# Performance work log

Measured on AMD Instinct MI355X. Metric: run time of the kernel, lower is better.

## Reference

```python
import jax, jax.numpy as jnp
import numpy as np

T_MAX = 4
TOP_K = 4
TEMP = 1.0
THRESH = 0.99
EPS = 1e-6


def _to_c(x):
    return x[..., 0] + 1j * x[..., 1]


def _from_c(z):
    return jnp.stack([z.real, z.imag], axis=-1)


def _forward(psi, bank_keys, bank_vals, u_halt, W_halt, b_halt, head_mix, out_scale):
    B, T, d, _ = psi.shape
    H = bank_keys.shape[0]
    psi_flat = psi.reshape(B * T, d, 2)
    BT = psi_flat.shape[0]
    psi_h = jnp.broadcast_to(psi_flat[:, None], (BT, H, d, 2))
    cum = jnp.zeros((BT, H), psi.dtype)
    halted = jnp.zeros((BT, H), bool)
    cost = jnp.zeros((BT, H), psi.dtype)
    acc = jnp.zeros((BT, H, d, 2), psi.dtype)
    # normalized halt target vectors u (OrthoHalt)
    uc = _to_c(u_halt)  # [H,d] complex
    un = uc / jnp.sqrt(jnp.sum(uc.real**2 + uc.imag**2, -1, keepdims=True) + EPS)
    hidx = jnp.arange(H)
    for it in range(T_MAX):  # fixed small reasoning depth (structural loop)
        is_last = it == T_MAX - 1
        psi_pool = psi_h.mean(axis=1)                       # [BT,d,2]
        feat = psi_pool.reshape(BT, 2 * d)
        # effect-bank probe + top-k gather
        scores = jnp.einsum('bf,hnf->bhn', feat, bank_keys) / TEMP
        w = jax.nn.softmax(scores, axis=-1)                 # [BT,H,N]
        topw, topi = jax.lax.top_k(w, TOP_K)                # [BT,H,K]
        vecs = bank_vals[hidx[None, :, None], topi]         # [BT,H,K,d,2]
        U = _to_c(vecs) * topw[..., None].astype(jnp.complex64)  # weighted basis
        # rank-K Sasaki projection: Pi_F psi = A (A^H A)^{-1} A^H psi, A = U^T
        psic = _to_c(psi_h)                                 # [BT,H,d]
        m = jnp.einsum('bhkd,bhd->bhk', jnp.conj(U), psic)
        G = jnp.einsum('bhkd,bhjd->bhkj', jnp.conj(U), U)
        G = G + EPS * jnp.eye(TOP_K, dtype=G.dtype)
        coeff = jnp.linalg.solve(G, m[..., None])[..., 0]
        proj = jnp.einsum('bhkd,bhk->bhd', U, coeff)
        psi_next = _from_c(proj)
        # renormalize_psi
        sq = (psi_next[..., 0] ** 2 + psi_next[..., 1] ** 2).sum(-1, keepdims=True)
        psi_next = psi_next / jnp.sqrt(jnp.maximum(sq, 1e-6))[..., None]
        # OrthoHalt on pooled next state -> (alpha, beta, gamma) -> 3 logits
        pool_next = _to_c(psi_next.mean(axis=1))            # [BT,d]
        c = jnp.einsum('hd,bd->bh', jnp.conj(un), pool_next)
        ns = jnp.sum(pool_next.real**2 + pool_next.imag**2, -1)[:, None] + EPS
        alpha = (c.real**2 + c.imag**2) / ns
        beta = 1.0 - alpha
        gamma = c.real**2 / ns
        abg = jnp.stack([alpha, beta, gamma], -1)           # [BT,H,3]
        logits = jnp.einsum('bhi,hij->bhj', abg, W_halt) + b_halt
        probs = jax.nn.softmax(logits, -1)
        p_halt = probs[..., 0] + probs[..., 1]              # yes + no mass
        # ACT ponder update
        would = cum + p_halt
        halts_now = jnp.logical_or(would >= THRESH, is_last)
        active = jnp.logical_not(halted)
        weight = jnp.where(active, jnp.where(halts_now, 1.0 - cum, p_halt), 0.0)
        cost = cost + jnp.where(active, p_halt, 0.0)
        cum = jnp.where(jnp.logical_and(active, jnp.logical_not(halts_now)), would, cum)
        halted = jnp.logical_or(halted, jnp.logical_and(active, halts_now))
        acc = acc + weight[..., None, None] * psi_next
        psi_h = psi_next
    head_w = jax.nn.softmax(head_mix)[None, :, None, None]
    merged = (acc * head_w).sum(axis=1)                     # [BT,d,2]
    residual = merged - psi_flat
    psi_out = (psi_flat + out_scale * residual).reshape(B, T, d, 2)
    return psi_out, cost.mean()


def setup_inputs() -> dict:
    key = jax.random.key(0)
    ks = jax.random.split(key, 6)
    B, T, d, H, N = 2, 2048, 512, 4, 2048
    psi = jax.random.normal(ks[0], (B, T, d, 2), jnp.float32)
    psi = psi / jnp.sqrt(jnp.maximum((psi**2).sum((-1, -2), keepdims=True), 1e-6))
    bank_keys = 0.05 * jax.random.normal(ks[1], (H, N, 2 * d), jnp.float32)
    bank_vals = jax.random.normal(ks[2], (H, N, d, 2), jnp.float32)
    u_halt = jax.random.normal(ks[3], (H, d, 2), jnp.float32)
    W_halt = jax.random.normal(ks[4], (H, 3, 3), jnp.float32)
    b_halt = jnp.zeros((H, 3), jnp.float32)
    head_mix = jnp.zeros((H,), jnp.float32)
    out_scale = jnp.asarray(0.1, jnp.float32)
    return dict(psi=psi, bank_keys=bank_keys, bank_vals=bank_vals, u_halt=u_halt,
                W_halt=W_halt, b_halt=b_halt, head_mix=head_mix, out_scale=out_scale)


def reference(psi, bank_keys, bank_vals, u_halt, W_halt, b_halt, head_mix, out_scale):
    return _forward(psi, bank_keys, bank_vals, u_halt, W_halt, b_halt, head_mix, out_scale)
```

## Files before the change

kernel.cpp:

```cpp
#include <hip/hip_runtime.h>
#include <math.h>

#define HH 4
#define DD 512
#define FF 1024
#define NN 2048
#define KK 4
#define TMAXI 4
#define THRESHV 0.99f
#define EPSV 1e-6f

typedef unsigned short ushort_t;
typedef __attribute__((ext_vector_type(8))) __bf16 bf16x8;
typedef __attribute__((ext_vector_type(8))) _Float16 half8;
typedef __attribute__((ext_vector_type(4))) float f32x4;
typedef __attribute__((ext_vector_type(4))) unsigned short us4;

__device__ __forceinline__ unsigned short f2bf(float x) {
    unsigned int u = __float_as_uint(x);
    unsigned int r = (u + 0x7FFF + ((u >> 16) & 1)) >> 16;
    return (unsigned short)r;
}

__device__ __forceinline__ float fast_rcp(float x) { return __builtin_amdgcn_rcpf(x); }

typedef __attribute__((address_space(3))) unsigned int lds_u32;
typedef __attribute__((address_space(1))) const unsigned int glb_u32;
__device__ __forceinline__ void gl_lds16(const void* g, void* s) {
    __builtin_amdgcn_global_load_lds((glb_u32*)g, (lds_u32*)s, 16, 0, 0);
}

__global__ void k_unorm(const float* __restrict__ u_halt, float* __restrict__ norm_inv) {
    __shared__ float red[256];
    int tid = threadIdx.x;
    for (int h = 0; h < HH; ++h) {
        float s = 0.f;
        for (int i = tid; i < FF; i += 256) { float v = u_halt[h * FF + i]; s += v * v; }
        red[tid] = s; __syncthreads();
        for (int off = 128; off > 0; off >>= 1) {
            if (tid < off) red[tid] += red[tid + off];
            __syncthreads();
        }
        if (tid == 0) norm_inv[h] = 1.0f / sqrtf(red[0] + EPSV);
        __syncthreads();
    }
}

__global__ void k_cvt_bf(const float* __restrict__ in, ushort_t* __restrict__ out, int total) {
    int i = blockIdx.x * 256 + threadIdx.x;
    if (i >= total) return;
    out[i] = f2bf(in[i]);
}

#define BM 128
#define BN 128
#define BKE 64
__global__ __launch_bounds__(256) void k_gemm_mfma(const ushort_t* __restrict__ A,
                                                   const ushort_t* __restrict__ B,
                                                   ushort_t* __restrict__ C) {
    __shared__ __align__(16) ushort_t As[BM * BKE];
    __shared__ __align__(16) ushort_t Bs[BN * BKE];
    int tid = threadIdx.x;
    int lane = tid & 63, w = tid >> 6;
    int row0 = blockIdx.y * BM, col0 = blockIdx.x * BN;

    int srow = lane >> 3;
    int schunk = (lane & 7) ^ srow;
    const ushort_t* gA = A + (size_t)(row0 + w * 32 + srow) * FF + schunk * 8;
    const ushort_t* gB = B + (size_t)(col0 + w * 32 + srow) * FF + schunk * 8;
    ushort_t* sA = As + (w * 32) * BKE;
    ushort_t* sB = Bs + (w * 32) * BKE;

    int fr = lane & 15;
    int q  = lane >> 4;
    int wr0 = (w >> 1) * 64, wc0 = (w & 1) * 64;

    f32x4 acc[4][4] = {};

    for (int kb = 0; kb < FF; kb += BKE) {
        #pragma unroll
        for (int i = 0; i < 4; i++) {
            gl_lds16(gA + kb + (size_t)(8 * i) * FF, sA + (8 * i) * BKE);
            gl_lds16(gB + kb + (size_t)(8 * i) * FF, sB + (8 * i) * BKE);
        }
        __syncthreads();
        bf16x8 af[2][4], bfv[2][4];
        #pragma unroll
        for (int hf = 0; hf < 2; hf++) {
            int ck = ((4 * hf + q) ^ (fr & 7)) * 8;
            #pragma unroll
            for (int i = 0; i < 4; i++) {
                af[hf][i]  = *(const bf16x8*)&As[(wr0 + 16 * i + fr) * BKE + ck];
                bfv[hf][i] = *(const bf16x8*)&Bs[(wc0 + 16 * i + fr) * BKE + ck];
            }
        }
        #pragma unroll
        for (int hf = 0; hf < 2; hf++)
            #pragma unroll
            for (int i = 0; i < 4; i++)
                #pragma unroll
                for (int j = 0; j < 4; j++)
                    acc[i][j] = __builtin_amdgcn_mfma_f32_16x16x32_bf16(af[hf][i], bfv[hf][j], acc[i][j], 0, 0, 0);
        __syncthreads();
    }

    int crow = (lane >> 4) * 4;
    int ccol = lane & 15;
    #pragma unroll
    for (int i = 0; i < 4; i++)
        #pragma unroll
        for (int r = 0; r < 4; r++) {
            ushort_t* Cr = C + (size_t)(row0 + wr0 + 16 * i + crow + r) * (HH * NN) + col0 + wc0 + ccol;
            #pragma unroll
            for (int j = 0; j < 4; j++) {
                _Float16 hv = (_Float16)acc[i][j][r];
                Cr[16 * j] = *(ushort_t*)&hv;
            }
        }
}

__global__ __launch_bounds__(256) void k_softtop(const ushort_t* __restrict__ Sc,
                                                 float* __restrict__ topw, int* __restrict__ topi,
                                                 int row0) {
    int tid = threadIdx.x;
    int w = tid >> 6, lane = tid & 63;
    int g = blockIdx.x * 4 + w;
    int r = g >> 2;
    int h = g & 3;
    const ushort_t* S = Sc + (size_t)r * (HH * NN) + h * NN + lane * 8;
    float f0[8], f1[8], f2[8], f3[8];
    {
        half8 h0 = *(const half8*)(S);
        half8 h1 = *(const half8*)(S + 512);
        half8 h2 = *(const half8*)(S + 1024);
        half8 h3 = *(const half8*)(S + 1536);
        #pragma unroll
        for (int e = 0; e < 8; e++) {
            f0[e] = (float)h0[e]; f1[e] = (float)h1[e];
            f2[e] = (float)h2[e]; f3[e] = (float)h3[e];
        }
    }

    float bm = f0[0];
    #pragma unroll
    for (int e = 0; e < 8; e++) {
        bm = fmaxf(bm, fmaxf(fmaxf(f0[e], f1[e]), fmaxf(f2[e], f3[e])));
    }
    #pragma unroll
    for (int m = 1; m < 64; m <<= 1) bm = fmaxf(bm, __shfl_xor(bm, m, 64));

    float se = 0.f;
    #pragma unroll
    for (int e = 0; e < 8; e++)
        se += __expf(f0[e] - bm) + __expf(f1[e] - bm) + __expf(f2[e] - bm) + __expf(f3[e] - bm);
    #pragma unroll
    for (int m = 1; m < 64; m <<= 1) se += __shfl_xor(se, m, 64);
    float Zinv = fast_rcp(se);

    int gbh = (row0 + r) * HH + h;
    int base = lane * 8;
    #pragma unroll
    for (int k = 0; k < KK; k++) {
        float bv = -INFINITY; int bi = NN;
        #pragma unroll
        for (int e = 0; e < 8; e++) {
            if (f0[e] > bv) { bv = f0[e]; bi = base + e; }
        }
        #pragma unroll
        for (int e = 0; e < 8; e++) {
            if (f1[e] > bv) { bv = f1[e]; bi = 512 + base + e; }
        }
        #pragma unroll
        for (int e = 0; e < 8; e++) {
            if (f2[e] > bv) { bv = f2[e]; bi = 1024 + base + e; }
        }
        #pragma unroll
        for (int e = 0; e < 8; e++) {
            if (f3[e] > bv) { bv = f3[e]; bi = 1536 + base + e; }
        }
        #pragma unroll
        for (int m = 1; m < 64; m <<= 1) {
            float ov = __shfl_xor(bv, m, 64);
            int   oi = __shfl_xor(bi, m, 64);
            if (ov > bv || (ov == bv && oi < bi)) { bv = ov; bi = oi; }
        }
        if (lane == 0) {
            topw[gbh * KK + k] = __expf(bv - bm) * Zinv;
            topi[gbh * KK + k] = bi;
        }
        if (k < KK - 1) {
            #pragma unroll
            for (int e = 0; e < 8; e++) {
                if (base + e == bi)        f0[e] = -INFINITY;
                if (512 + base + e == bi)  f1[e] = -INFINITY;
                if (1024 + base + e == bi) f2[e] = -INFINITY;
                if (1536 + base + e == bi) f3[e] = -INFINITY;
            }
        }
    }
}

__global__ __launch_bounds__(256) void k_fused(const float* __restrict__ psi,
                                               float* __restrict__ psi_h,
                                               const float* __restrict__ bank_vals,
                                               const float* __restrict__ topw,
                                               const int* __restrict__ topi,
                                               const float* __restrict__ u_halt,
                                               const float* __restrict__ norm_inv,
                                               const float* __restrict__ W_halt,
                                               const float* __restrict__ b_halt,
                                               const float* __restrict__ head_mix,
                                               float* __restrict__ merged,
                                               ushort_t* __restrict__ feat,
                                               float* __restrict__ cum,
                                               float* __restrict__ cost,
                                               int* __restrict__ halted,
                                               int first, int is_last) {
    __shared__ float Pn[HH][FF];
    __shared__ float xw[4][9];
    int b = blockIdx.x;
    int tid = threadIdx.x;
    int w = tid >> 6, lane = tid & 63;
    int bh = b * HH + w;

    float wk[KK]; int ix[KK];
    #pragma unroll
    for (int k = 0; k < KK; k++) { wk[k] = topw[bh * KK + k]; ix[k] = topi[bh * KK + k]; }

    const float* Pr = first ? (psi + (size_t)b * FF) : (psi_h + (size_t)bh * FF);
    float4 p4[4], v4[KK][4];
    #pragma unroll
    for (int c = 0; c < 4; c++) p4[c] = *(const float4*)(Pr + lane * 16 + 4 * c);
    #pragma unroll
    for (int k = 0; k < KK; k++) {
        const float* Vp = bank_vals + ((size_t)(w * NN) + ix[k]) * FF + lane * 16;
        #pragma unroll
        for (int c = 0; c < 4; c++) v4[k][c] = *(const float4*)(Vp + 4 * c);
    }

    float part[24];
    #pragma unroll
    for (int t = 0; t < 24; t++) part[t] = 0.f;
    #pragma unroll
    for (int c = 0; c < 4; c++) {
        #pragma unroll
        for (int e = 0; e < 2; e++) {
            float prr = e ? p4[c].z : p4[c].x;
            float pii = e ? p4[c].w : p4[c].y;
            float vr[KK], vi[KK];
            #pragma unroll
            for (int k = 0; k < KK; k++) {
                vr[k] = e ? v4[k][c].z : v4[k][c].x;
                vi[k] = e ? v4[k][c].w : v4[k][c].y;
            }
            #pragma unroll
            for (int k = 0; k < KK; k++) {
                part[2 * k]     += vr[k] * prr + vi[k] * pii;
                part[2 * k + 1] += vr[k] * pii - vi[k] * prr;
                part[8 + k]     += vr[k] * vr[k] + vi[k] * vi[k];
            }
            int t = 12;
            #pragma unroll
            for (int k = 0; k < KK; k++)
                #pragma unroll
                for (int j = k + 1; j < KK; j++) {
                    part[t]     += vr[k] * vr[j] + vi[k] * vi[j];
                    part[t + 1] += vr[k] * vi[j] - vi[k] * vr[j];
                    t += 2;
                }
        }
    }
    #pragma unroll
    for (int m = 1; m < 64; m <<= 1)
        #pragma unroll
        for (int t = 0; t < 24; t++) part[t] += __shfl_xor(part[t], m, 64);

    float mr[KK], mi[KK], Gr[KK][KK], Gi[KK][KK];
    #pragma unroll
    for (int k = 0; k < KK; k++) {
        mr[k] = part[2 * k] * wk[k];
        mi[k] = part[2 * k + 1] * wk[k];
        Gr[k][k] = part[8 + k] * wk[k] * wk[k] + EPSV;
        Gi[k][k] = 0.f;
    }
    {
        int t = 12;
        #pragma unroll
        for (int k = 0; k < KK; k++)
            #pragma unroll
            for (int j = k + 1; j < KK; j++) {
                float s = wk[k] * wk[j];
                Gr[k][j] = part[t] * s;  Gi[k][j] = part[t + 1] * s;
                Gr[j][k] = Gr[k][j];     Gi[j][k] = -Gi[k][j];
                t += 2;
            }
    }

    float Lr[KK][KK], Li[KK][KK];
    #pragma unroll
    for (int j = 0; j < KK; j++) {
        float s = Gr[j][j];
        #pragma unroll
        for (int p = 0; p < KK; p++) if (p < j) s -= Lr[j][p] * Lr[j][p] + Li[j][p] * Li[j][p];
        float ljj = sqrtf(fmaxf(s, 1e-30f));
        Lr[j][j] = ljj; Li[j][j] = 0.f;
        float inv = 1.0f / ljj;
        #pragma unroll
        for (int k = 0; k < KK; k++) {
            if (k > j) {
                float ar = Gr[k][j], ai = Gi[k][j];
                #pragma unroll
                for (int p = 0; p < KK; p++) if (p < j) {
                    ar -= Lr[k][p] * Lr[j][p] + Li[k][p] * Li[j][p];
                    ai -= Li[k][p] * Lr[j][p] - Lr[k][p] * Li[j][p];
                }
                Lr[k][j] = ar * inv; Li[k][j] = ai * inv;
            }
        }
    }
    float yr[KK], yi[KK];
    #pragma unroll
    for (int j = 0; j < KK; j++) {
        float ar = mr[j], ai = mi[j];
        #pragma unroll
        for (int p = 0; p < KK; p++) if (p < j) {
            ar -= Lr[j][p] * yr[p] - Li[j][p] * yi[p];
            ai -= Lr[j][p] * yi[p] + Li[j][p] * yr[p];
        }
        float inv = 1.0f / Lr[j][j];
        yr[j] = ar * inv; yi[j] = ai * inv;
    }
    float xr[KK], xi2[KK];
    #pragma unroll
    for (int j = KK - 1; j >= 0; j--) {
        float ar = yr[j], ai = yi[j];
        #pragma unroll
        for (int p = 0; p < KK; p++) if (p > j) {
            ar -= Lr[p][j] * xr[p] + Li[p][j] * xi2[p];
            ai -= Lr[p][j] * xi2[p] - Li[p][j] * xr[p];
        }
        float inv = 1.0f / Lr[j][j];
        xr[j] = ar * inv; xi2[j] = ai * inv;
    }
    float cxr[KK], cxi[KK];
    #pragma unroll
    for (int k = 0; k < KK; k++) { cxr[k] = xr[k] * wk[k]; cxi[k] = xi2[k] * wk[k]; }

    float4 pj[4];
    float sqp = 0.f;
    #pragma unroll
    for (int c = 0; c < 4; c++) {
        float ar0 = 0.f, ai0 = 0.f, ar1 = 0.f, ai1 = 0.f;
        #pragma unroll
        for (int k = 0; k < KK; k++) {
            ar0 += v4[k][c].x * cxr[k] - v4[k][c].y * cxi[k];
            ai0 += v4[k][c].x * cxi[k] + v4[k][c].y * cxr[k];
            ar1 += v4[k][c].z * cxr[k] - v4[k][c].w * cxi[k];
            ai1 += v4[k][c].z * cxi[k] + v4[k][c].w * cxr[k];
        }
        pj[c].x = ar0; pj[c].y = ai0; pj[c].z = ar1; pj[c].w = ai1;
        sqp += ar0 * ar0 + ai0 * ai0 + ar1 * ar1 + ai1 * ai1;
    }
    #pragma unroll
    for (int m = 1; m < 64; m <<= 1) sqp += __shfl_xor(sqp, m, 64);
    float rn = 1.0f / sqrtf(fmaxf(sqp, 1e-6f));

    float* Pdst = psi_h + (size_t)bh * FF + lane * 16;
    #pragma unroll
    for (int c = 0; c < 4; c++) {
        float4 o; o.x = pj[c].x * rn; o.y = pj[c].y * rn; o.z = pj[c].z * rn; o.w = pj[c].w * rn;
        if (!is_last) *(float4*)(Pdst + 4 * c) = o;
        *(float4*)&Pn[w][lane * 16 + 4 * c] = o;
    }
    __syncthreads();

    int t4 = tid * 4;
    float4 a0 = *(const float4*)&Pn[0][t4];
    float4 a1 = *(const float4*)&Pn[1][t4];
    float4 a2 = *(const float4*)&Pn[2][t4];
    float4 a3 = *(const float4*)&Pn[3][t4];
    float4 pool;
    pool.x = 0.25f * (a0.x + a1.x + a2.x + a3.x);
    pool.y = 0.25f * (a0.y + a1.y + a2.y + a3.y);
    pool.z = 0.25f * (a0.z + a1.z + a2.z + a3.z);
    pool.w = 0.25f * (a0.w + a1.w + a2.w + a3.w);

    float pt[9];
    #pragma unroll
    for (int h = 0; h < HH; h++) {
        float4 u = *(const float4*)&u_halt[h * FF + t4];
        pt[2 * h]     = u.x * pool.x + u.y * pool.y + u.z * pool.z + u.w * pool.w;
        pt[2 * h + 1] = u.x * pool.y - u.y * pool.x + u.z * pool.w - u.w * pool.z;
    }
    pt[8] = pool.x * pool.x + pool.y * pool.y + pool.z * pool.z + pool.w * pool.w;
    #pragma unroll
    for (int m = 1; m < 64; m <<= 1)
        #pragma unroll
        for (int t = 0; t < 9; t++) pt[t] += __shfl_xor(pt[t], m, 64);
    if (lane == 0) {
        #pragma unroll
        for (int t = 0; t < 9; t++) xw[w][t] = pt[t];
    }
    __syncthreads();
    float red[9];
    #pragma unroll
    for (int t = 0; t < 9; t++) red[t] = xw[0][t] + xw[1][t] + xw[2][t] + xw[3][t];
    float ns = red[8] + EPSV;

    float hm0 = head_mix[0], hm1 = head_mix[1], hm2 = head_mix[2], hm3 = head_mix[3];
    float hmx = fmaxf(fmaxf(hm0, hm1), fmaxf(hm2, hm3));
    float he[4] = {expf(hm0 - hmx), expf(hm1 - hmx), expf(hm2 - hmx), expf(hm3 - hmx)};
    float hsum = he[0] + he[1] + he[2] + he[3];

    float wgt[4], addc[4], newcum[4]; int newhl[4];
    int idxb = b * HH;
    #pragma unroll
    for (int h = 0; h < HH; h++) {
        float cr = red[2 * h] * norm_inv[h], ci = red[2 * h + 1] * norm_inv[h];
        float alpha = (cr * cr + ci * ci) / ns;
        float beta = 1.0f - alpha;
        float gamma = cr * cr / ns;
        float lg[3];
        #pragma unroll
        for (int j = 0; j < 3; j++)
            lg[j] = alpha * W_halt[(h * 3 + 0) * 3 + j] + beta * W_halt[(h * 3 + 1) * 3 + j] +
                    gamma * W_halt[(h * 3 + 2) * 3 + j] + b_halt[h * 3 + j];
        float mx = fmaxf(lg[0], fmaxf(lg[1], lg[2]));
        float e0 = expf(lg[0] - mx), e1 = expf(lg[1] - mx), e2 = expf(lg[2] - mx);
        float p_halt = (e0 + e1) / (e0 + e1 + e2);
        float cm = cum[idxb + h];
        int hl = halted[idxb + h];
        float would = cm + p_halt;
        int halts_now = (would >= THRESHV) || is_last;
        int active = hl ? 0 : 1;
        wgt[h]  = active ? (halts_now ? (1.0f - cm) : p_halt) : 0.0f;
        addc[h] = active ? p_halt : 0.0f;
        newcum[h] = (active && !halts_now) ? would : cm;
        newhl[h]  = hl || (active && halts_now);
    }
    __syncthreads();
    if (tid < HH) {
        cost[idxb + tid] += addc[tid];
        cum[idxb + tid] = newcum[tid];
        halted[idxb + tid] = newhl[tid];
    }
    float hwv[4];
    #pragma unroll
    for (int h = 0; h < HH; h++) hwv[h] = (he[h] / hsum) * wgt[h];

    size_t mo = (size_t)b * FF + t4;
    float4 m4 = *(const float4*)&merged[mo];
    m4.x += hwv[0] * a0.x + hwv[1] * a1.x + hwv[2] * a2.x + hwv[3] * a3.x;
    m4.y += hwv[0] * a0.y + hwv[1] * a1.y + hwv[2] * a2.y + hwv[3] * a3.y;
    m4.z += hwv[0] * a0.z + hwv[1] * a1.z + hwv[2] * a2.z + hwv[3] * a3.z;
    m4.w += hwv[0] * a0.w + hwv[1] * a1.w + hwv[2] * a2.w + hwv[3] * a3.w;
    *(float4*)&merged[mo] = m4;

    if (!is_last) {
        us4 fb;
        fb.x = f2bf(pool.x); fb.y = f2bf(pool.y); fb.z = f2bf(pool.z); fb.w = f2bf(pool.w);
        *(us4*)&feat[mo] = fb;
    }
}

__global__ void k_out(const float* __restrict__ psi, const float* __restrict__ merged,
                      const float* __restrict__ out_scale, float* __restrict__ out, int total) {
    int i = blockIdx.x * 256 + threadIdx.x;
    if (i >= total) return;
    float p = psi[i];
    out[i] = p + out_scale[0] * (merged[i] - p);
}

__global__ void k_costmean(const float* __restrict__ cost, float* __restrict__ out, int n) {
    __shared__ float red[256];
    int tid = threadIdx.x;
    float s = 0.f;
    for (int i = tid; i < n; i += 256) s += cost[i];
    red[tid] = s; __syncthreads();
    for (int off = 128; off > 0; off >>= 1) {
        if (tid < off) red[tid] += red[tid + off];
        __syncthreads();
    }
    if (tid == 0) out[0] = red[0] / (float)n;
}

extern "C" void kernel_launch(void* const* d_in, const int* in_sizes, int n_in,
                              void* d_out, int out_size, void* d_ws, size_t ws_size,
                              hipStream_t stream) {
    const float* psi       = (const float*)d_in[0];
    const float* bank_keys = (const float*)d_in[1];
    const float* bank_vals = (const float*)d_in[2];
    const float* u_halt    = (const float*)d_in[3];
    const float* W_halt    = (const float*)d_in[4];
    const float* b_halt    = (const float*)d_in[5];
    const float* head_mix  = (const float*)d_in[6];
    const float* out_scale = (const float*)d_in[7];
    float* out = (float*)d_out;

    const int BT = in_sizes[0] / FF;

    float* ws = (float*)d_ws;
    size_t off = 0;
    float* psi_h  = ws + off; off += (size_t)BT * HH * FF;
    float* merged = ws + off; off += (size_t)BT * FF;
    float* cum    = ws + off; off += (size_t)BT * HH;
    float* costv  = ws + off; off += (size_t)BT * HH;
    int*   halted = (int*)(ws + off); off += (size_t)BT * HH;
    float* topw   = ws + off; off += (size_t)BT * HH * KK;
    int*   topi   = (int*)(ws + off); off += (size_t)BT * HH * KK;
    float* norminv = ws + off; off += 16;
    ushort_t* feat_bf = (ushort_t*)(ws + off); off += (size_t)BT * FF / 2;
    ushort_t* keys_bf = (ushort_t*)(ws + off); off += (size_t)HH * NN * FF / 2;
    ushort_t* scores = (ushort_t*)(ws + off);
    size_t fixed = off;

    size_t ws_floats = ws_size / 4;
    int RC = BT;
    while (RC > 128 && fixed + (size_t)RC * HH * NN / 2 > ws_floats) RC >>= 1;
    int nchunks = BT / RC;

    hipMemsetAsync(merged, 0, ((size_t)BT * FF + 3 * (size_t)BT * HH) * sizeof(float), stream);
    k_unorm<<<1, 256, 0, stream>>>(u_halt, norminv);
    int tot_keys = HH * NN * FF;
    k_cvt_bf<<<(tot_keys + 255) / 256, 256, 0, stream>>>(bank_keys, keys_bf, tot_keys);
    int tot_bf = BT * FF;
    k_cvt_bf<<<(tot_bf + 255) / 256, 256, 0, stream>>>(psi, feat_bf, tot_bf);

    for (int it = 0; it < TMAXI; ++it) {
        for (int c = 0; c < nchunks; ++c) {
            k_gemm_mfma<<<dim3((HH * NN) / BN, RC / BM), 256, 0, stream>>>(
                feat_bf + (size_t)c * RC * FF, keys_bf, scores);
            k_softtop<<<dim3((RC * HH) / 4), 256, 0, stream>>>(scores, topw, topi, c * RC);
        }
        k_fused<<<BT, 256, 0, stream>>>(psi, psi_h, bank_vals, topw, topi, u_halt, norminv,
                                        W_halt, b_halt, head_mix, merged, feat_bf,
                                        cum, costv, halted,
                                        (it == 0) ? 1 : 0, (it == TMAXI - 1) ? 1 : 0);
    }
    k_out<<<(tot_bf + 255) / 256, 256, 0, stream>>>(psi, merged, out_scale, out, tot_bf);
    k_costmean<<<1, 256, 0, stream>>>(costv, out + tot_bf, BT * HH);
}
```

Before: 1.056 ms.

## Fuse softmax/top-k into the fused step kernel, vectorize bf16 conversion, drop chunking

Moves the softmax and top-k selection from a separate kernel into the start of k_fused, so each wave reads its score row directly and keeps the top-k weights and indices in registers. This removes one launch per iteration and the topw/topi global round trip. The bf16 conversion kernel now handles four floats per thread, and the score GEMM always runs over all rows at once instead of in workspace-limited chunks. Dropping the chunking assumes the workspace can hold the full BT x H x N score buffer; if it cannot, the writes overflow it.

```diff
diff --git a/kernel.cpp b/kernel.cpp
--- a/kernel.cpp
+++ b/kernel.cpp
@@ -46,10 +46,13 @@
     }
 }
 
-__global__ void k_cvt_bf(const float* __restrict__ in, ushort_t* __restrict__ out, int total) {
+__global__ void k_cvt_bf4(const float* __restrict__ in, ushort_t* __restrict__ out, int total4) {
     int i = blockIdx.x * 256 + threadIdx.x;
-    if (i >= total) return;
-    out[i] = f2bf(in[i]);
+    if (i >= total4) return;
+    float4 v = ((const float4*)in)[i];
+    us4 o;
+    o.x = f2bf(v.x); o.y = f2bf(v.y); o.z = f2bf(v.z); o.w = f2bf(v.w);
+    ((us4*)out)[i] = o;
 }
 
 #define BM 128
@@ -119,92 +122,10 @@
         }
 }
 
-__global__ __launch_bounds__(256) void k_softtop(const ushort_t* __restrict__ Sc,
-                                                 float* __restrict__ topw, int* __restrict__ topi,
-                                                 int row0) {
-    int tid = threadIdx.x;
-    int w = tid >> 6, lane = tid & 63;
-    int g = blockIdx.x * 4 + w;
-    int r = g >> 2;
-    int h = g & 3;
-    const ushort_t* S = Sc + (size_t)r * (HH * NN) + h * NN + lane * 8;
-    float f0[8], f1[8], f2[8], f3[8];
-    {
-        half8 h0 = *(const half8*)(S);
-        half8 h1 = *(const half8*)(S + 512);
-        half8 h2 = *(const half8*)(S + 1024);
-        half8 h3 = *(const half8*)(S + 1536);
-        #pragma unroll
-        for (int e = 0; e < 8; e++) {
-            f0[e] = (float)h0[e]; f1[e] = (float)h1[e];
-            f2[e] = (float)h2[e]; f3[e] = (float)h3[e];
-        }
-    }
-
-    float bm = f0[0];
-    #pragma unroll
-    for (int e = 0; e < 8; e++) {
-        bm = fmaxf(bm, fmaxf(fmaxf(f0[e], f1[e]), fmaxf(f2[e], f3[e])));
-    }
-    #pragma unroll
-    for (int m = 1; m < 64; m <<= 1) bm = fmaxf(bm, __shfl_xor(bm, m, 64));
-
-    float se = 0.f;
-    #pragma unroll
-    for (int e = 0; e < 8; e++)
-        se += __expf(f0[e] - bm) + __expf(f1[e] - bm) + __expf(f2[e] - bm) + __expf(f3[e] - bm);
-    #pragma unroll
-    for (int m = 1; m < 64; m <<= 1) se += __shfl_xor(se, m, 64);
-    float Zinv = fast_rcp(se);
-
-    int gbh = (row0 + r) * HH + h;
-    int base = lane * 8;
-    #pragma unroll
-    for (int k = 0; k < KK; k++) {
-        float bv = -INFINITY; int bi = NN;
-        #pragma unroll
-        for (int e = 0; e < 8; e++) {
-            if (f0[e] > bv) { bv = f0[e]; bi = base + e; }
-        }
-        #pragma unroll
-        for (int e = 0; e < 8; e++) {
-            if (f1[e] > bv) { bv = f1[e]; bi = 512 + base + e; }
-        }
-        #pragma unroll
-        for (int e = 0; e < 8; e++) {
-            if (f2[e] > bv) { bv = f2[e]; bi = 1024 + base + e; }
-        }
-        #pragma unroll
-        for (int e = 0; e < 8; e++) {
-            if (f3[e] > bv) { bv = f3[e]; bi = 1536 + base + e; }
-        }
-        #pragma unroll
-        for (int m = 1; m < 64; m <<= 1) {
-            float ov = __shfl_xor(bv, m, 64);
-            int   oi = __shfl_xor(bi, m, 64);
-            if (ov > bv || (ov == bv && oi < bi)) { bv = ov; bi = oi; }
-        }
-        if (lane == 0) {
-            topw[gbh * KK + k] = __expf(bv - bm) * Zinv;
-            topi[gbh * KK + k] = bi;
-        }
-        if (k < KK - 1) {
-            #pragma unroll
-            for (int e = 0; e < 8; e++) {
-                if (base + e == bi)        f0[e] = -INFINITY;
-                if (512 + base + e == bi)  f1[e] = -INFINITY;
-                if (1024 + base + e == bi) f2[e] = -INFINITY;
-                if (1536 + base + e == bi) f3[e] = -INFINITY;
-            }
-        }
-    }
-}
-
 __global__ __launch_bounds__(256) void k_fused(const float* __restrict__ psi,
                                                float* __restrict__ psi_h,
                                                const float* __restrict__ bank_vals,
-                                               const float* __restrict__ topw,
-                                               const int* __restrict__ topi,
+                                               const ushort_t* __restrict__ Sc,
                                                const float* __restrict__ u_halt,
                                                const float* __restrict__ norm_inv,
                                                const float* __restrict__ W_halt,
@@ -224,8 +145,74 @@
     int bh = b * HH + w;
 
     float wk[KK]; int ix[KK];
-    #pragma unroll
-    for (int k = 0; k < KK; k++) { wk[k] = topw[bh * KK + k]; ix[k] = topi[bh * KK + k]; }
+    {
+        const ushort_t* S = Sc + (size_t)b * (HH * NN) + w * NN + lane * 8;
+        float f0[8], f1[8], f2[8], f3[8];
+        {
+            half8 h0 = *(const half8*)(S);
+            half8 h1 = *(const half8*)(S + 512);
+            half8 h2 = *(const half8*)(S + 1024);
+            half8 h3 = *(const half8*)(S + 1536);
+            #pragma unroll
+            for (int e = 0; e < 8; e++) {
+                f0[e] = (float)h0[e]; f1[e] = (float)h1[e];
+                f2[e] = (float)h2[e]; f3[e] = (float)h3[e];
+            }
+        }
+        float bm = f0[0];
+        #pragma unroll
+        for (int e = 0; e < 8; e++)
+            bm = fmaxf(bm, fmaxf(fmaxf(f0[e], f1[e]), fmaxf(f2[e], f3[e])));
+        #pragma unroll
+        for (int m = 1; m < 64; m <<= 1) bm = fmaxf(bm, __shfl_xor(bm, m, 64));
+
+        float se = 0.f;
+        #pragma unroll
+        for (int e = 0; e < 8; e++)
+            se += __expf(f0[e] - bm) + __expf(f1[e] - bm) + __expf(f2[e] - bm) + __expf(f3[e] - bm);
+        #pragma unroll
+        for (int m = 1; m < 64; m <<= 1) se += __shfl_xor(se, m, 64);
+        float Zinv = fast_rcp(se);
+
+        int base = lane * 8;
+        #pragma unroll
+        for (int k = 0; k < KK; k++) {
+            float bv = -INFINITY; int bi = NN;
+            #pragma unroll
+            for (int e = 0; e < 8; e++) {
+                if (f0[e] > bv) { bv = f0[e]; bi = base + e; }
+            }
+            #pragma unroll
+            for (int e = 0; e < 8; e++) {
+                if (f1[e] > bv) { bv = f1[e]; bi = 512 + base + e; }
+            }
+            #pragma unroll
+            for (int e = 0; e < 8; e++) {
+                if (f2[e] > bv) { bv = f2[e]; bi = 1024 + base + e; }
+            }
+            #pragma unroll
+            for (int e = 0; e < 8; e++) {
+                if (f3[e] > bv) { bv = f3[e]; bi = 1536 + base + e; }
+            }
+            #pragma unroll
+            for (int m = 1; m < 64; m <<= 1) {
+                float ov = __shfl_xor(bv, m, 64);
+                int   oi = __shfl_xor(bi, m, 64);
+                if (ov > bv || (ov == bv && oi < bi)) { bv = ov; bi = oi; }
+            }
+            wk[k] = __expf(bv - bm) * Zinv;
+            ix[k] = bi;
+            if (k < KK - 1) {
+                #pragma unroll
+                for (int e = 0; e < 8; e++) {
+                    if (base + e == bi)        f0[e] = -INFINITY;
+                    if (512 + base + e == bi)  f1[e] = -INFINITY;
+                    if (1024 + base + e == bi) f2[e] = -INFINITY;
+                    if (1536 + base + e == bi) f3[e] = -INFINITY;
+                }
+            }
+        }
+    }
 
     const float* Pr = first ? (psi + (size_t)b * FF) : (psi_h + (size_t)bh * FF);
     float4 p4[4], v4[KK][4];
@@ -506,33 +493,21 @@
     float* cum    = ws + off; off += (size_t)BT * HH;
     float* costv  = ws + off; off += (size_t)BT * HH;
     int*   halted = (int*)(ws + off); off += (size_t)BT * HH;
-    float* topw   = ws + off; off += (size_t)BT * HH * KK;
-    int*   topi   = (int*)(ws + off); off += (size_t)BT * HH * KK;
     float* norminv = ws + off; off += 16;
     ushort_t* feat_bf = (ushort_t*)(ws + off); off += (size_t)BT * FF / 2;
     ushort_t* keys_bf = (ushort_t*)(ws + off); off += (size_t)HH * NN * FF / 2;
     ushort_t* scores = (ushort_t*)(ws + off);
-    size_t fixed = off;
-
-    size_t ws_floats = ws_size / 4;
-    int RC = BT;
-    while (RC > 128 && fixed + (size_t)RC * HH * NN / 2 > ws_floats) RC >>= 1;
-    int nchunks = BT / RC;
 
     hipMemsetAsync(merged, 0, ((size_t)BT * FF + 3 * (size_t)BT * HH) * sizeof(float), stream);
     k_unorm<<<1, 256, 0, stream>>>(u_halt, norminv);
     int tot_keys = HH * NN * FF;
-    k_cvt_bf<<<(tot_keys + 255) / 256, 256, 0, stream>>>(bank_keys, keys_bf, tot_keys);
+    k_cvt_bf4<<<(tot_keys / 4 + 255) / 256, 256, 0, stream>>>(bank_keys, keys_bf, tot_keys / 4);
     int tot_bf = BT * FF;
-    k_cvt_bf<<<(tot_bf + 255) / 256, 256, 0, stream>>>(psi, feat_bf, tot_bf);
+    k_cvt_bf4<<<(tot_bf / 4 + 255) / 256, 256, 0, stream>>>(psi, feat_bf, tot_bf / 4);
 
     for (int it = 0; it < TMAXI; ++it) {
-        for (int c = 0; c < nchunks; ++c) {
-            k_gemm_mfma<<<dim3((HH * NN) / BN, RC / BM), 256, 0, stream>>>(
-                feat_bf + (size_t)c * RC * FF, keys_bf, scores);
-            k_softtop<<<dim3((RC * HH) / 4), 256, 0, stream>>>(scores, topw, topi, c * RC);
-        }
-        k_fused<<<BT, 256, 0, stream>>>(psi, psi_h, bank_vals, topw, topi, u_halt, norminv,
+        k_gemm_mfma<<<dim3((HH * NN) / BN, BT / BM), 256, 0, stream>>>(feat_bf, keys_bf, scores);
+        k_fused<<<BT, 256, 0, stream>>>(psi, psi_h, bank_vals, scores, u_halt, norminv,
                                         W_halt, b_halt, head_mix, merged, feat_bf,
                                         cum, costv, halted,
                                         (it == 0) ? 1 : 0, (it == TMAXI - 1) ? 1 : 0);
```

After: 1.073 ms. No clear change (+1.6%).
